# Kernel optimization log

Hardware: AMD Instinct MI355X
Metric: run time of the kernel (lower is better)

Reference implementation:

```python
import jax, jax.numpy as jnp
import numpy as np

ALPHA, BETA, GAMMA = 1.0, 0.5, 0.3
EPS = 1e-08


def setup_inputs() -> dict:
    key = jax.random.key(0)
    k1, k2, k3, k4, k5 = jax.random.split(key, 5)
    B, C, F = 32, 256, 2048
    return {
        "mag_hat": jax.random.normal(k1, (B, C, F), dtype=jnp.float32),
        "phase_hat": jax.random.normal(k2, (B, C, F), dtype=jnp.float32),
        "mag_target": jax.random.normal(k3, (B, C, F), dtype=jnp.float32),
        "phase_target": jax.random.normal(k4, (B, C, F), dtype=jnp.float32),
        "pci_target": jax.random.uniform(k5, (B, C, C), dtype=jnp.float32),
    }


def _pci(phase):
    # phase: (B, C, F). Naive form is mean_f cos/sin(phi_i - phi_j) over a
    # (B,C,C,F) broadcast; rewrite with cos(a-b)=ca*cb+sa*sb and
    # sin(a-b)=sa*cb-ca*sb as two batched GEMMs on (C,F) matrices.
    c = jnp.cos(phase)
    s = jnp.sin(phase)
    inv_f = 1.0 / phase.shape[-1]
    real = (jnp.einsum('bif,bjf->bij', c, c) + jnp.einsum('bif,bjf->bij', s, s)) * inv_f
    imag = (jnp.einsum('bif,bjf->bij', s, c) - jnp.einsum('bif,bjf->bij', c, s)) * inv_f
    return jnp.sqrt(real * real + imag * imag + EPS)


def reference(mag_hat, phase_hat, mag_target, phase_target, pci_target):
    mag_loss = jnp.mean((mag_hat - mag_target) ** 2)
    phase_loss = jnp.mean(1.0 - jnp.cos(phase_hat - phase_target))
    pci_hat = _pci(phase_hat)
    coh_loss = jnp.mean((pci_hat - pci_target) ** 2)
    total = ALPHA * mag_loss + BETA * phase_loss + GAMMA * coh_loss
    return (total, mag_loss, phase_loss, coh_loss)
```

## Files before the change

### kernel.cpp

```cpp
#include <hip/hip_runtime.h>
#include <hip/hip_bf16.h>

#define ALPHA_ 1.0f
#define BETA_  0.5f
#define GAMMA_ 0.3f
#define EPS_   1e-8f

typedef unsigned short u16;
typedef unsigned int u32;

constexpr int B_ = 32, C_ = 256, F_ = 2048;
constexpr int NTOT = B_ * C_ * F_;
constexpr int NCC  = B_ * C_ * C_;
constexpr int NPOS = 10;
constexpr int KSPL = 4;
constexpr int NBLK = B_ * NPOS * KSPL;
constexpr int NRED = B_ * NPOS * 64 * 64;

__constant__ int TI_[NPOS] = {0, 1, 2, 3, 0, 0, 0, 1, 1, 2};
__constant__ int TJ_[NPOS] = {0, 1, 2, 3, 1, 2, 3, 2, 3, 3};

typedef __bf16 bf16x8 __attribute__((ext_vector_type(8)));
typedef float  f32x4  __attribute__((ext_vector_type(4)));

__device__ __forceinline__ u32 f2bf(float x) {
    unsigned u = __float_as_uint(x);
    u += 0x7fffu + ((u >> 16) & 1u);
    return (u >> 16);
}

__global__ void __launch_bounds__(256)
ew_kernel(const float4* __restrict__ mh, const float4* __restrict__ ph,
          const float4* __restrict__ mt, const float4* __restrict__ pt,
          float* __restrict__ part)
{
    __shared__ float sm[4], sp[4];
    const int g = blockIdx.x * 256 + threadIdx.x;
    float4 p = ph[g], q = pt[g], a = mh[g], b = mt[g];

    float msum = 0.f, psum = 0.f;
    float dm;
    dm = a.x - b.x; msum += dm * dm; psum += 1.f - __cosf(p.x - q.x);
    dm = a.y - b.y; msum += dm * dm; psum += 1.f - __cosf(p.y - q.y);
    dm = a.z - b.z; msum += dm * dm; psum += 1.f - __cosf(p.z - q.z);
    dm = a.w - b.w; msum += dm * dm; psum += 1.f - __cosf(p.w - q.w);

    #pragma unroll
    for (int o = 32; o > 0; o >>= 1) {
        msum += __shfl_down(msum, o, 64);
        psum += __shfl_down(psum, o, 64);
    }
    int lane = threadIdx.x & 63, wv = threadIdx.x >> 6;
    if (lane == 0) { sm[wv] = msum; sp[wv] = psum; }
    __syncthreads();
    if (threadIdx.x == 0) {
        int slot = blockIdx.x & 63;
        atomicAdd(&part[slot],      sm[0] + sm[1] + sm[2] + sm[3]);
        atomicAdd(&part[64 + slot], sp[0] + sp[1] + sp[2] + sp[3]);
    }
}

__device__ __forceinline__ void stage8(float4 a, float4 b, char* base, int pc) {
    float v[8] = {a.x, a.y, a.z, a.w, b.x, b.y, b.z, b.w};
    u32 cu[8], su[8];
    #pragma unroll
    for (int j = 0; j < 8; j++) {
        float s, c;
        __sincosf(v[j], &s, &c);
        cu[j] = f2bf(c);
        su[j] = f2bf(s);
    }
    *(int4*)(base + pc) = make_int4(
        (int)(cu[0] | (cu[1] << 16)), (int)(cu[2] | (cu[3] << 16)),
        (int)(cu[4] | (cu[5] << 16)), (int)(cu[6] | (cu[7] << 16)));
    *(int4*)(base + (pc ^ 128)) = make_int4(
        (int)(su[0] | (su[1] << 16)), (int)(su[2] | (su[3] << 16)),
        (int)(su[4] | (su[5] << 16)), (int)(su[6] | (su[7] << 16)));
}

__global__ void __launch_bounds__(256)
pci_kernel(const float* __restrict__ ph, float* __restrict__ slabs)
{
    __shared__ char lds[32768];
    char* la = lds;
    char* lb = lds + 16384;

    const int bid = blockIdx.x;
    const int l   = (bid & 7) * (NBLK / 8) + (bid >> 3);
    const int h   = l & 3;
    const int t4  = l >> 2;
    const int pos = t4 % NPOS;
    const int y   = t4 / NPOS;
    const int i0 = TI_[pos] * 64, j0 = TJ_[pos] * 64;
    const bool diag = (i0 == j0);
    char* lbp = diag ? la : lb;

    const int t    = threadIdx.x;
    const int lane = t & 63, w = t >> 6;
    const int wrow = (w >> 1) * 32, wcol = (w & 1) * 32;
    const int m = lane & 15, q = lane >> 4;

    const int row0 = t >> 3, oct = t & 7;
    const int row1 = row0 + 32;
    const float* gA0 = ph + ((size_t)(y * 256 + i0 + row0) * 2048 + h * 512 + oct * 8);
    const float* gA1 = ph + ((size_t)(y * 256 + i0 + row1) * 2048 + h * 512 + oct * 8);
    const float* gB0 = ph + ((size_t)(y * 256 + j0 + row0) * 2048 + h * 512 + oct * 8);
    const float* gB1 = ph + ((size_t)(y * 256 + j0 + row1) * 2048 + h * 512 + oct * 8);
    char* dA0 = la + row0 * 256;  const int pc0 = (oct ^ (row0 & 15)) * 16;
    char* dA1 = la + row1 * 256;  const int pc1 = (oct ^ (row1 & 15)) * 16;
    char* dB0 = lb + row0 * 256;
    char* dB1 = lb + row1 * 256;

    f32x4 zero = {0.f, 0.f, 0.f, 0.f};
    f32x4 accR[2][2], accSC[2][2], accCS[2][2];
    #pragma unroll
    for (int a = 0; a < 2; a++)
        #pragma unroll
        for (int c = 0; c < 2; c++) {
            accR[a][c] = zero; accSC[a][c] = zero; accCS[a][c] = zero;
        }

    for (int it = 0; it < 8; ++it) {
        __syncthreads();
        float4 a0 = *(const float4*)gA0, a1 = *(const float4*)(gA0 + 4);
        float4 a2 = *(const float4*)gA1, a3 = *(const float4*)(gA1 + 4);
        float4 b0, b1, b2, b3;
        if (!diag) {
            b0 = *(const float4*)gB0; b1 = *(const float4*)(gB0 + 4);
            b2 = *(const float4*)gB1; b3 = *(const float4*)(gB1 + 4);
        }
        gA0 += 64; gA1 += 64; gB0 += 64; gB1 += 64;
        stage8(a0, a1, dA0, pc0);
        stage8(a2, a3, dA1, pc1);
        if (!diag) {
            stage8(b0, b1, dB0, pc0);
            stage8(b2, b3, dB1, pc1);
        }
        __syncthreads();

        #pragma unroll
        for (int s = 0; s < 2; ++s) {
            bf16x8 fac[2], fas[2], fbc[2], fbs[2];
            #pragma unroll
            for (int a = 0; a < 2; a++) {
                const char* base = la + (wrow + a * 16 + m) * 256;
                int pc = ((4 * s + q) ^ m) * 16;
                fac[a] = *(const bf16x8*)(base + pc);
                fas[a] = *(const bf16x8*)(base + (pc ^ 128));
            }
            #pragma unroll
            for (int c = 0; c < 2; c++) {
                const char* base = lbp + (wcol + c * 16 + m) * 256;
                int pc = ((4 * s + q) ^ m) * 16;
                fbc[c] = *(const bf16x8*)(base + pc);
                fbs[c] = *(const bf16x8*)(base + (pc ^ 128));
            }
            #pragma unroll
            for (int a = 0; a < 2; a++)
                #pragma unroll
                for (int c = 0; c < 2; c++) {
                    accR[a][c]  = __builtin_amdgcn_mfma_f32_16x16x32_bf16(fac[a], fbc[c], accR[a][c], 0, 0, 0);
                    accR[a][c]  = __builtin_amdgcn_mfma_f32_16x16x32_bf16(fas[a], fbs[c], accR[a][c], 0, 0, 0);
                    accSC[a][c] = __builtin_amdgcn_mfma_f32_16x16x32_bf16(fas[a], fbc[c], accSC[a][c], 0, 0, 0);
                    accCS[a][c] = __builtin_amdgcn_mfma_f32_16x16x32_bf16(fac[a], fbs[c], accCS[a][c], 0, 0, 0);
                }
        }
    }

    float* sl = slabs + (size_t)h * ((size_t)NRED * 2)
                      + (size_t)(y * NPOS + pos) * 8192;
    #pragma unroll
    for (int a = 0; a < 2; a++)
        #pragma unroll
        for (int c = 0; c < 2; c++) {
            int ii = wrow + a * 16 + q * 4;
            int jj = wcol + c * 16 + m;
            #pragma unroll
            for (int r = 0; r < 4; r++) {
                int idx = (ii + r) * 64 + jj;
                float2 v = make_float2(accR[a][c][r], accSC[a][c][r] - accCS[a][c][r]);
                *(float2*)(sl + (size_t)idx * 2) = v;
            }
        }
}

__global__ void __launch_bounds__(256)
coh_kernel(const float* __restrict__ slabs, const float* __restrict__ tgt,
           float* __restrict__ accum)
{
    __shared__ float pl[64 * 65];
    __shared__ float sred[4];
    const int blk = blockIdx.x;
    const int y   = blk / NPOS;
    const int pos = blk % NPOS;
    const int t   = threadIdx.x;
    const bool off = (pos >= 4);
    const float invf = 1.0f / (float)F_;
    const int ib = TI_[pos] * 64, jb = TJ_[pos] * 64;
    const float* ty = tgt + (size_t)y * (C_ * C_);
    const size_t sb0 = (size_t)(y * NPOS + pos) * 8192;

    float coh = 0.f;
    #pragma unroll
    for (int k = 0; k < 8; ++k) {
        int e = 2 * t + k * 512;
        float r0 = 0.f, s0 = 0.f, r1 = 0.f, s1 = 0.f;
        #pragma unroll
        for (int hh = 0; hh < 4; ++hh) {
            float4 v = *(const float4*)(slabs
                + (size_t)hh * ((size_t)NRED * 2) + sb0 + (size_t)e * 2);
            r0 += v.x; s0 += v.y; r1 += v.z; s1 += v.w;
        }
        float re0 = r0 * invf, im0 = s0 * invf;
        float re1 = r1 * invf, im1 = s1 * invf;
        float p0 = sqrtf(re0 * re0 + im0 * im0 + EPS_);
        float p1 = sqrtf(re1 * re1 + im1 * im1 + EPS_);
        int ii = e >> 6, jj = e & 63;
        pl[ii * 65 + jj]     = p0;
        pl[ii * 65 + jj + 1] = p1;
        float2 tg = *(const float2*)(ty + (size_t)(ib + ii) * C_ + jb + jj);
        float d0 = p0 - tg.x, d1 = p1 - tg.y;
        coh += d0 * d0 + d1 * d1;
    }
    __syncthreads();

    if (off) {
        #pragma unroll
        for (int k = 0; k < 8; ++k) {
            int e = 2 * t + k * 512;
            int ii = e >> 6, jj = e & 63;
            float p0 = pl[jj * 65 + ii];
            float p1 = pl[(jj + 1) * 65 + ii];
            float2 tg = *(const float2*)(ty + (size_t)(jb + ii) * C_ + ib + jj);
            float d0 = p0 - tg.x, d1 = p1 - tg.y;
            coh += d0 * d0 + d1 * d1;
        }
    }

    #pragma unroll
    for (int o = 32; o > 0; o >>= 1) coh += __shfl_down(coh, o, 64);
    int lane = t & 63, w = t >> 6;
    if (lane == 0) sred[w] = coh;
    __syncthreads();
    if (t == 0)
        atomicAdd(&accum[2], sred[0] + sred[1] + sred[2] + sred[3]);
}

__global__ void fin_kernel(const float* __restrict__ accum,
                           const float* __restrict__ part,
                           float* __restrict__ out)
{
    int t = threadIdx.x;
    float m = part[t], p = part[64 + t];
    #pragma unroll
    for (int o = 32; o > 0; o >>= 1) {
        m += __shfl_down(m, o, 64);
        p += __shfl_down(p, o, 64);
    }
    if (t == 0) {
        float mag = m * (1.0f / (float)NTOT);
        float phs = p * (1.0f / (float)NTOT);
        float coh = accum[2] * (1.0f / (float)NCC);
        out[0] = ALPHA_ * mag + BETA_ * phs + GAMMA_ * coh;
        out[1] = mag;
        out[2] = phs;
        out[3] = coh;
    }
}

extern "C" void kernel_launch(void* const* d_in, const int* in_sizes, int n_in,
                              void* d_out, int out_size, void* d_ws, size_t ws_size,
                              hipStream_t stream)
{
    const float* mh  = (const float*)d_in[0];
    const float* ph  = (const float*)d_in[1];
    const float* mt  = (const float*)d_in[2];
    const float* pt  = (const float*)d_in[3];
    const float* tgt = (const float*)d_in[4];
    float* out = (float*)d_out;

    float* accum = (float*)d_ws;
    float* part  = (float*)((char*)d_ws + 256);
    float* slabs = (float*)((char*)d_ws + 1024);

    hipMemsetAsync(d_ws, 0, 1024, stream);

    ew_kernel<<<16384, 256, 0, stream>>>(
        (const float4*)mh, (const float4*)ph, (const float4*)mt, (const float4*)pt,
        part);

    pci_kernel<<<NBLK, 256, 0, stream>>>(ph, slabs);

    coh_kernel<<<320, 256, 0, stream>>>(slabs, tgt, accum);

    fin_kernel<<<1, 64, 0, stream>>>(accum, part, out);
}
```

Measured before the change: 314.6 us.

## Fuse phase loss into PCI kernel diagonal blocks and prefetch next tile

The phase-loss term is now computed inside the PCI GEMM kernel: diagonal-tile blocks, which already load every phase_hat row once, also load phase_target and accumulate 1-cos differences. This removes one full read of phase_hat from the elementwise pass, which now handles only the magnitude loss with 8 elements per thread. The PCI main loop also prefetches the next iteration's global loads into registers before the MFMA work. The cost is more register pressure and extra load work concentrated in the diagonal blocks, which adds imbalance across blocks.

```diff
diff --git a/kernel.cpp b/kernel.cpp
--- a/kernel.cpp
+++ b/kernel.cpp
@@ -30,34 +30,31 @@
 }
 
 __global__ void __launch_bounds__(256)
-ew_kernel(const float4* __restrict__ mh, const float4* __restrict__ ph,
-          const float4* __restrict__ mt, const float4* __restrict__ pt,
-          float* __restrict__ part)
-{
-    __shared__ float sm[4], sp[4];
+mag_kernel(const float4* __restrict__ mh, const float4* __restrict__ mt,
+           float* __restrict__ part)
+{
+    __shared__ float sm[4];
     const int g = blockIdx.x * 256 + threadIdx.x;
-    float4 p = ph[g], q = pt[g], a = mh[g], b = mt[g];
-
-    float msum = 0.f, psum = 0.f;
-    float dm;
-    dm = a.x - b.x; msum += dm * dm; psum += 1.f - __cosf(p.x - q.x);
-    dm = a.y - b.y; msum += dm * dm; psum += 1.f - __cosf(p.y - q.y);
-    dm = a.z - b.z; msum += dm * dm; psum += 1.f - __cosf(p.z - q.z);
-    dm = a.w - b.w; msum += dm * dm; psum += 1.f - __cosf(p.w - q.w);
-
-    #pragma unroll
-    for (int o = 32; o > 0; o >>= 1) {
-        msum += __shfl_down(msum, o, 64);
-        psum += __shfl_down(psum, o, 64);
-    }
+    float4 a0 = mh[2*g], a1 = mh[2*g+1];
+    float4 b0 = mt[2*g], b1 = mt[2*g+1];
+
+    float msum = 0.f, dm;
+    dm = a0.x - b0.x; msum += dm * dm;
+    dm = a0.y - b0.y; msum += dm * dm;
+    dm = a0.z - b0.z; msum += dm * dm;
+    dm = a0.w - b0.w; msum += dm * dm;
+    dm = a1.x - b1.x; msum += dm * dm;
+    dm = a1.y - b1.y; msum += dm * dm;
+    dm = a1.z - b1.z; msum += dm * dm;
+    dm = a1.w - b1.w; msum += dm * dm;
+
+    #pragma unroll
+    for (int o = 32; o > 0; o >>= 1) msum += __shfl_down(msum, o, 64);
     int lane = threadIdx.x & 63, wv = threadIdx.x >> 6;
-    if (lane == 0) { sm[wv] = msum; sp[wv] = psum; }
+    if (lane == 0) sm[wv] = msum;
     __syncthreads();
-    if (threadIdx.x == 0) {
-        int slot = blockIdx.x & 63;
-        atomicAdd(&part[slot],      sm[0] + sm[1] + sm[2] + sm[3]);
-        atomicAdd(&part[64 + slot], sp[0] + sp[1] + sp[2] + sp[3]);
-    }
+    if (threadIdx.x == 0)
+        atomicAdd(&part[blockIdx.x & 63], sm[0] + sm[1] + sm[2] + sm[3]);
 }
 
 __device__ __forceinline__ void stage8(float4 a, float4 b, char* base, int pc) {
@@ -78,10 +75,25 @@
         (int)(su[4] | (su[5] << 16)), (int)(su[6] | (su[7] << 16)));
 }
 
+__device__ __forceinline__ float phs8(float4 a, float4 b, float4 qa, float4 qb) {
+    float s = 0.f;
+    s += 1.f - __cosf(a.x - qa.x);
+    s += 1.f - __cosf(a.y - qa.y);
+    s += 1.f - __cosf(a.z - qa.z);
+    s += 1.f - __cosf(a.w - qa.w);
+    s += 1.f - __cosf(b.x - qb.x);
+    s += 1.f - __cosf(b.y - qb.y);
+    s += 1.f - __cosf(b.z - qb.z);
+    s += 1.f - __cosf(b.w - qb.w);
+    return s;
+}
+
 __global__ void __launch_bounds__(256)
-pci_kernel(const float* __restrict__ ph, float* __restrict__ slabs)
+pci_kernel(const float* __restrict__ ph, const float* __restrict__ pt,
+           float* __restrict__ slabs, float* __restrict__ part)
 {
     __shared__ char lds[32768];
+    __shared__ float sred[4];
     char* la = lds;
     char* lb = lds + 16384;
 
@@ -102,10 +114,14 @@
 
     const int row0 = t >> 3, oct = t & 7;
     const int row1 = row0 + 32;
-    const float* gA0 = ph + ((size_t)(y * 256 + i0 + row0) * 2048 + h * 512 + oct * 8);
-    const float* gA1 = ph + ((size_t)(y * 256 + i0 + row1) * 2048 + h * 512 + oct * 8);
+    const size_t offA0 = (size_t)(y * 256 + i0 + row0) * 2048 + h * 512 + oct * 8;
+    const size_t offA1 = (size_t)(y * 256 + i0 + row1) * 2048 + h * 512 + oct * 8;
+    const float* gA0 = ph + offA0;
+    const float* gA1 = ph + offA1;
     const float* gB0 = ph + ((size_t)(y * 256 + j0 + row0) * 2048 + h * 512 + oct * 8);
     const float* gB1 = ph + ((size_t)(y * 256 + j0 + row1) * 2048 + h * 512 + oct * 8);
+    const float* gQ0 = pt + offA0;
+    const float* gQ1 = pt + offA1;
     char* dA0 = la + row0 * 256;  const int pc0 = (oct ^ (row0 & 15)) * 16;
     char* dA1 = la + row1 * 256;  const int pc1 = (oct ^ (row1 & 15)) * 16;
     char* dB0 = lb + row0 * 256;
@@ -120,23 +136,45 @@
             accR[a][c] = zero; accSC[a][c] = zero; accCS[a][c] = zero;
         }
 
+    float psum = 0.f;
+    float4 a0 = *(const float4*)gA0, a1 = *(const float4*)(gA0 + 4);
+    float4 a2 = *(const float4*)gA1, a3 = *(const float4*)(gA1 + 4);
+    float4 b0, b1, b2, b3, q0, q1, q2, q3;
+    if (diag) {
+        q0 = *(const float4*)gQ0; q1 = *(const float4*)(gQ0 + 4);
+        q2 = *(const float4*)gQ1; q3 = *(const float4*)(gQ1 + 4);
+    } else {
+        b0 = *(const float4*)gB0; b1 = *(const float4*)(gB0 + 4);
+        b2 = *(const float4*)gB1; b3 = *(const float4*)(gB1 + 4);
+    }
+    gA0 += 64; gA1 += 64; gB0 += 64; gB1 += 64; gQ0 += 64; gQ1 += 64;
+
     for (int it = 0; it < 8; ++it) {
         __syncthreads();
-        float4 a0 = *(const float4*)gA0, a1 = *(const float4*)(gA0 + 4);
-        float4 a2 = *(const float4*)gA1, a3 = *(const float4*)(gA1 + 4);
-        float4 b0, b1, b2, b3;
-        if (!diag) {
-            b0 = *(const float4*)gB0; b1 = *(const float4*)(gB0 + 4);
-            b2 = *(const float4*)gB1; b3 = *(const float4*)(gB1 + 4);
-        }
-        gA0 += 64; gA1 += 64; gB0 += 64; gB1 += 64;
         stage8(a0, a1, dA0, pc0);
         stage8(a2, a3, dA1, pc1);
-        if (!diag) {
+        if (diag) {
+            psum += phs8(a0, a1, q0, q1);
+            psum += phs8(a2, a3, q2, q3);
+        } else {
             stage8(b0, b1, dB0, pc0);
             stage8(b2, b3, dB1, pc1);
         }
         __syncthreads();
+
+        if (it < 7) {
+            a0 = *(const float4*)gA0; a1 = *(const float4*)(gA0 + 4);
+            a2 = *(const float4*)gA1; a3 = *(const float4*)(gA1 + 4);
+            if (diag) {
+                q0 = *(const float4*)gQ0; q1 = *(const float4*)(gQ0 + 4);
+                q2 = *(const float4*)gQ1; q3 = *(const float4*)(gQ1 + 4);
+            } else {
+                b0 = *(const float4*)gB0; b1 = *(const float4*)(gB0 + 4);
+                b2 = *(const float4*)gB1; b3 = *(const float4*)(gB1 + 4);
+            }
+            gA0 += 64; gA1 += 64; gB0 += 64; gB1 += 64; gQ0 += 64; gQ1 += 64;
+            __builtin_amdgcn_sched_barrier(0);
+        }
 
         #pragma unroll
         for (int s = 0; s < 2; ++s) {
@@ -182,6 +220,15 @@
                 *(float2*)(sl + (size_t)idx * 2) = v;
             }
         }
+
+    if (diag) {
+        #pragma unroll
+        for (int o = 32; o > 0; o >>= 1) psum += __shfl_down(psum, o, 64);
+        if (lane == 0) sred[w] = psum;
+        __syncthreads();
+        if (t == 0)
+            atomicAdd(&part[64 + (bid & 63)], sred[0] + sred[1] + sred[2] + sred[3]);
+    }
 }
 
 __global__ void __launch_bounds__(256)
@@ -285,11 +332,10 @@
 
     hipMemsetAsync(d_ws, 0, 1024, stream);
 
-    ew_kernel<<<16384, 256, 0, stream>>>(
-        (const float4*)mh, (const float4*)ph, (const float4*)mt, (const float4*)pt,
-        part);
-
-    pci_kernel<<<NBLK, 256, 0, stream>>>(ph, slabs);
+    mag_kernel<<<8192, 256, 0, stream>>>(
+        (const float4*)mh, (const float4*)mt, part);
+
+    pci_kernel<<<NBLK, 256, 0, stream>>>(ph, pt, slabs, part);
 
     coh_kernel<<<320, 256, 0, stream>>>(slabs, tgt, accum);
 
```

After: 287.6 us. 8.6% less time.
